# Kernel tuning notes

Measured on AMD Instinct MI355X. Metric: run time of the kernel, lower is better.

## Reference

```python
import jax, jax.numpy as jnp
import numpy as np

SHIFTS = (1, 2)          # _GLOBAL_SHIFTS, all < channels so none filtered
LN_EPS = 1e-5


def _layernorm(x, g, b):
    mu = jnp.mean(x, axis=-1, keepdims=True)
    var = jnp.var(x, axis=-1, keepdims=True)
    return (x - mu) * jax.lax.rsqrt(var + LN_EPS) * g + b


def setup_inputs() -> dict:
    key = jax.random.key(0)
    ks = jax.random.split(key, 4)
    B, H, W, D = 8, 96, 96, 256
    n_comp = 2 * len(SHIFTS)  # full mode: dot + wedge per shift
    x = jax.random.normal(ks[0], (B, H, W, D), dtype=jnp.float32)
    # glorot-uniform style scaling for the two dense kernels
    pk = jax.random.normal(ks[1], (n_comp * D, D), dtype=jnp.float32) * (1.0 / np.sqrt(n_comp * D))
    gk = jax.random.normal(ks[2], (2 * D, D), dtype=jnp.float32) * (1.0 / np.sqrt(2 * D))
    return {
        "x": x,
        "ln_gamma": jnp.ones((D,), jnp.float32),
        "ln_beta": jnp.zeros((D,), jnp.float32),
        "proj_kernel": pk,
        "proj_bias": jnp.zeros((D,), jnp.float32),
        "gate_kernel": gk,
        "gate_bias": jnp.zeros((D,), jnp.float32),
        "gamma": jnp.full((D,), 1e-5, jnp.float32),  # LayerScale init
    }


def reference(x, ln_gamma, ln_beta, proj_kernel, proj_bias,
              gate_kernel, gate_bias, gamma):
    # ---- pre-norm ----
    h_norm = _layernorm(x, ln_gamma, ln_beta)                 # [B,H,W,D]
    # ---- context stream (ctx_mode='diff'): deviation from spatial mean ----
    z_det = h_norm
    z_ctx = h_norm - jnp.mean(h_norm, axis=(1, 2), keepdims=True)
    # ---- sparse rolling Clifford product (cli_mode='full') ----
    feats = []
    for s in SHIFTS:
        ctx_s = jnp.roll(z_ctx, -s, axis=-1)   # Z_ctx[(c+s) % D]
        det_s = jnp.roll(z_det, -s, axis=-1)   # Z_det[(c+s) % D]
        dot = jax.nn.silu(z_det * ctx_s)                      # inner part
        wedge = z_det * ctx_s - z_ctx * det_s                 # bivector part
        feats.append(dot)
        feats.append(wedge)
    feats = jnp.concatenate(feats, axis=-1)                   # [B,H,W,4D]
    g_feat = feats @ proj_kernel + proj_bias                  # [B,H,W,D]
    # ---- gated geometric residual ----
    gate_in = jnp.concatenate([h_norm, g_feat], axis=-1)      # [B,H,W,2D]
    alpha = jax.nn.sigmoid(gate_in @ gate_kernel + gate_bias)
    h_mix = (jax.nn.silu(h_norm) + alpha * g_feat) * gamma    # LayerScale
    # drop_path_rate == 0.0 -> identity; caller-side residual add
    return x + h_mix
```

## Files before the change

kernel.cpp:

```cpp
#include <hip/hip_runtime.h>
#include <hip/hip_bf16.h>

typedef unsigned short u16;
typedef unsigned int   u32;
typedef __attribute__((ext_vector_type(4))) float f32x4;
typedef __attribute__((ext_vector_type(4))) u32   u32x4;
typedef __attribute__((ext_vector_type(8))) short bf16x8;

#define HWPIX  9216
#define NPIX   73728
#define LN_EPS 1e-5f
#define MROW   64
#define HSTR   264
#define ASTR   40

template<int N> struct IC { static constexpr int value = N; };

__device__ __forceinline__ u16 f2bf(float f){
  u32 u = __builtin_bit_cast(u32, f);
  u += 0x7fffu + ((u >> 16) & 1u);
  return (u16)(u >> 16);
}
__device__ __forceinline__ u32 pkbf(float lo, float hi){
  u32 d;
  asm("v_cvt_pk_bf16_f32 %0, %1, %2" : "=v"(d) : "v"(lo), "v"(hi));
  return d;
}
__device__ __forceinline__ float lo2f(u32 w){ return __builtin_bit_cast(float, w << 16); }
__device__ __forceinline__ float hi2f(u32 w){ return __builtin_bit_cast(float, w & 0xffff0000u); }
__device__ __forceinline__ float bfu2f(u16 h){ return __builtin_bit_cast(float, (u32)h << 16); }
__device__ __forceinline__ float fsigmoid(float v){ return __fdividef(1.f, 1.f + __expf(-v)); }
__device__ __forceinline__ float fsilu(float v){ return __fdividef(v, 1.f + __expf(-v)); }

__global__ __launch_bounds__(256) void wconv(const float* __restrict__ pk,
                                             const float* __restrict__ gk,
                                             u16* __restrict__ wsdot,
                                             u16* __restrict__ wsgate)
{
  int gid = blockIdx.x * 256 + threadIdx.x;
  int t = gid >> 10, S = gid & 1023;
  int q = (S >> 2) & 15, pp = S & 3, w8 = (S >> 6) & 7, rb = S >> 9;
  int n  = rb * 128 + w8 * 16 + q;
  int kq = pp ^ ((q >> 1) & 3);
  const float* W; int k0; u16* dst;
  if (t < 8)       { W = pk; k0 =       t      * 32 + kq * 8; dst = wsdot  + (size_t)t * 8192; }
  else if (t < 16) { W = pk; k0 = 512 + (t-8)  * 32 + kq * 8; dst = wsdot  + (size_t)t * 8192; }
  else             { W = gk; k0 =       (t-16) * 32 + kq * 8; dst = wsgate + (size_t)(t-16) * 8192; }
  u32 ow[4];
  #pragma unroll
  for (int e = 0; e < 4; ++e) {
    float f0 = W[(size_t)(k0 + 2*e)     * 256 + n];
    float f1 = W[(size_t)(k0 + 2*e + 1) * 256 + n];
    ow[e] = (u32)f2bf(f0) | ((u32)f2bf(f1) << 16);
  }
  *(u32x4*)(dst + (size_t)S * 8) = (u32x4){ow[0], ow[1], ow[2], ow[3]};
}

__global__ __launch_bounds__(256) void ln_partial(const float* __restrict__ x,
                                                  const float* __restrict__ g,
                                                  const float* __restrict__ bt,
                                                  float* __restrict__ partial)
{
  const int bh = blockIdx.x;
  const int tid = threadIdx.x;
  const int wv = tid >> 6, lane = tid & 63;
  const float* xrow = x + (size_t)bh * 96 * 256;
  __shared__ float red[4][256];

  f32x4 gv = *(const f32x4*)(g  + lane * 4);
  f32x4 bv = *(const f32x4*)(bt + lane * 4);
  f32x4 acc = {0.f, 0.f, 0.f, 0.f};

  for (int w = wv; w < 96; w += 4) {
    f32x4 v = *(const f32x4*)(xrow + w * 256 + lane * 4);
    float s  = v[0] + v[1] + v[2] + v[3];
    float s2 = v[0]*v[0] + v[1]*v[1] + v[2]*v[2] + v[3]*v[3];
    #pragma unroll
    for (int m = 1; m < 64; m <<= 1) { s += __shfl_xor(s, m); s2 += __shfl_xor(s2, m); }
    float mu  = s * (1.f / 256.f);
    float var = s2 * (1.f / 256.f) - mu * mu;
    float rs  = rsqrtf(var + LN_EPS);
    #pragma unroll
    for (int j = 0; j < 4; ++j) acc[j] += (v[j] - mu) * rs * gv[j] + bv[j];
  }
  *(f32x4*)(&red[wv][lane * 4]) = acc;
  __syncthreads();
  float s = red[0][tid] + red[1][tid] + red[2][tid] + red[3][tid];
  partial[(size_t)bh * 256 + tid] = s;
}

__global__ __launch_bounds__(256) void ln_mean(const float* __restrict__ partial,
                                               float* __restrict__ mean)
{
  int b = blockIdx.x, c = threadIdx.x;
  float s = 0.f;
  for (int h = 0; h < 96; ++h) s += partial[((size_t)b * 96 + h) * 256 + c];
  float m = s * (1.f / 9216.f);
  mean[b * 258 + c] = m;
  if (c < 2) mean[b * 258 + 256 + c] = m;
}

__global__ __launch_bounds__(256) void wfold(const float* __restrict__ pk,
                                             const float* __restrict__ meang,
                                             u16* __restrict__ wsW)
{
  __shared__ float msh[256];
  int gid = blockIdx.x * 256 + threadIdx.x;
  int chunk = gid >> 10;
  int b = chunk >> 3, j = chunk & 7;
  msh[threadIdx.x] = meang[b * 258 + threadIdx.x];
  __syncthreads();
  int S = gid & 1023;
  int q = (S >> 2) & 15, pp = S & 3, w8 = (S >> 6) & 7, rb = S >> 9;
  int n  = rb * 128 + w8 * 16 + q;
  int kq = pp ^ ((q >> 1) & 3);
  u32 ow[4];
  #pragma unroll
  for (int e = 0; e < 4; ++e) {
    float r[2];
    #pragma unroll
    for (int hh = 0; hh < 2; ++hh) {
      int c = j * 32 + kq * 8 + 2 * e + hh;
      int cm1 = (c + 255) & 255, cm2 = (c + 254) & 255;
      int cp1 = (c + 1) & 255,   cp2 = (c + 2) & 255;
      r[hh] = msh[cm1] * pk[(size_t)(256 + cm1) * 256 + n]
            - msh[cp1] * pk[(size_t)(256 + c)   * 256 + n]
            + msh[cm2] * pk[(size_t)(768 + cm2) * 256 + n]
            - msh[cp2] * pk[(size_t)(768 + c)   * 256 + n];
    }
    ow[e] = (u32)f2bf(r[0]) | ((u32)f2bf(r[1]) << 16);
  }
  *(u32x4*)(wsW + (size_t)chunk * 8192 + (size_t)S * 8) = (u32x4){ow[0], ow[1], ow[2], ow[3]};
}

__global__ __launch_bounds__(512, 4) void fused(
    const float* __restrict__ x,
    const float* __restrict__ lng, const float* __restrict__ lnb,
    const u16* __restrict__ wsdot, const u16* __restrict__ wsW,
    const u16* __restrict__ wsgate,
    const float* __restrict__ pbias, const float* __restrict__ gbias,
    const float* __restrict__ gamma, const float* __restrict__ meang,
    float* __restrict__ out)
{
  __shared__ u16 hn[MROW * HSTR];
  __shared__ u16 afg[2][MROW * ASTR];
  __shared__ u16 Bl [2][8192];
  __shared__ float msh[258];

  const int tid  = threadIdx.x;
  const long pix0 = (long)blockIdx.x * MROW;
  const int bat  = (int)(pix0 / HWPIX);

  if (tid < 258) msh[tid] = meang[bat * 258 + tid];

  const int wave = tid >> 6, lane = tid & 63;
  const int wr = wave & 1, wc = wave >> 1;
  const int fr = lane & 15, kq = lane >> 4;
  const int bswz = (kq ^ ((fr >> 1) & 3)) * 8;
  const int br = tid >> 3, bo = (tid & 7) * 4;

  f32x4 acc[2][4];
  #pragma unroll
  for (int i = 0; i < 2; ++i)
    #pragma unroll
    for (int j = 0; j < 4; ++j) acc[i][j] = (f32x4){0.f, 0.f, 0.f, 0.f};
  u32 gfp[2][4][2];
  float pbv[4];
  #pragma unroll
  for (int nt = 0; nt < 4; ++nt) pbv[nt] = pbias[wc * 64 + nt * 16 + fr];

  u32x4 breg0, breg1;
  auto sgptr = [&](auto SG) -> const u16* {
    constexpr int sg = decltype(SG)::value;
    if constexpr      (sg == 0) return wsdot;
    else if constexpr (sg == 1) return wsdot + 8 * 8192;
    else if constexpr (sg == 2) return wsW + (size_t)bat * 65536;
    else if constexpr (sg == 3) return wsgate;
    else                        return wsgate + 8 * 8192;
  };
  auto loadB = [&](auto SG, int jn) {
    const u16* src = sgptr(SG) + (size_t)jn * 8192 + tid * 8;
    breg0 = *(const u32x4*)(src);
    breg1 = *(const u32x4*)(src + 4096);
  };
  auto writeB = [&](int buf) {
    *(u32x4*)(&Bl[buf][tid * 8])        = breg0;
    *(u32x4*)(&Bl[buf][tid * 8 + 4096]) = breg1;
  };

  loadB(IC<0>{}, 0);

  {
    const int p = tid >> 3, o = tid & 7;
    const float* xp = x + (pix0 + p) * 256 + o * 32;
    f32x4 v[8];
    float s = 0.f, s2 = 0.f;
    #pragma unroll
    for (int i = 0; i < 8; ++i) {
      v[i] = *(const f32x4*)(xp + i * 4);
      #pragma unroll
      for (int j = 0; j < 4; ++j) { s += v[i][j]; s2 += v[i][j] * v[i][j]; }
    }
    s += __shfl_xor(s, 1); s2 += __shfl_xor(s2, 1);
    s += __shfl_xor(s, 2); s2 += __shfl_xor(s2, 2);
    s += __shfl_xor(s, 4); s2 += __shfl_xor(s2, 4);
    float mu  = s * (1.f / 256.f);
    float var = s2 * (1.f / 256.f) - mu * mu;
    float rs  = rsqrtf(var + LN_EPS);

    const float* gp = lng + o * 32;
    const float* bp = lnb + o * 32;
    u16* zd = hn + p * HSTR + o * 32;
    u32 pad_d = 0;
    #pragma unroll
    for (int i = 0; i < 8; ++i) {
      f32x4 gg = *(const f32x4*)(gp + i * 4);
      f32x4 bb = *(const f32x4*)(bp + i * 4);
      float h0 = (v[i][0] - mu) * rs * gg[0] + bb[0];
      float h1 = (v[i][1] - mu) * rs * gg[1] + bb[1];
      float h2 = (v[i][2] - mu) * rs * gg[2] + bb[2];
      float h3 = (v[i][3] - mu) * rs * gg[3] + bb[3];
      u32 d0 = pkbf(h0, h1);
      u32 d1 = pkbf(h2, h3);
      *(u32*)(zd + i * 4)     = d0;
      *(u32*)(zd + i * 4 + 2) = d1;
      if (i == 0) pad_d = d0;
    }
    if (o == 0) *(u32*)(hn + p * HSTR + 256) = pad_d;
  }

  auto featsD = [&](auto SC, int w, int buf) {
    constexpr int s = decltype(SC)::value;
    const int cc = w * 32 + bo;
    const u16* zp = hn + br * HSTR + cc;
    u32 a0 = *(const u32*)(zp);
    u32 a1 = *(const u32*)(zp + 2);
    u32 a2 = *(const u32*)(zp + 4);
    float h0 = lo2f(a0), h1 = hi2f(a0), h2 = lo2f(a1);
    float h3 = hi2f(a1), h4 = lo2f(a2), h5 = hi2f(a2);
    float m0 = msh[cc + s], m1 = msh[cc + s + 1];
    float m2 = msh[cc + s + 2], m3 = msh[cc + s + 3];
    float t0, t1, t2, t3;
    if constexpr (s == 1) { t0 = h1; t1 = h2; t2 = h3; t3 = h4; }
    else                  { t0 = h2; t1 = h3; t2 = h4; t3 = h5; }
    float r0 = fsilu(h0 * (t0 - m0));
    float r1 = fsilu(h1 * (t1 - m1));
    float r2 = fsilu(h2 * (t2 - m2));
    float r3 = fsilu(h3 * (t3 - m3));
    *(u32*)(&afg[buf][br * ASTR + bo])     = pkbf(r0, r1);
    *(u32*)(&afg[buf][br * ASTR + bo + 2]) = pkbf(r2, r3);
  };

  auto gfcopy = [&](auto CGC, int buf) {
    constexpr int cg = decltype(CGC)::value;
    constexpr int par = cg & 1;
    if (wc == (cg >> 1)) {
      #pragma unroll
      for (int v = 0; v < 2; ++v) {
        #pragma unroll
        for (int ai = 0; ai < 2; ++ai)
          #pragma unroll
          for (int rp = 0; rp < 2; ++rp) {
            u32 pw = gfp[ai][par * 2 + v][rp];
            int row0 = wr * 32 + ai * 16 + kq * 4 + rp * 2;
            afg[buf][row0 * ASTR + v * 16 + fr]       = (u16)pw;
            afg[buf][(row0 + 1) * ASTR + v * 16 + fr] = (u16)(pw >> 16);
          }
      }
    }
  };

  auto domfma = [&](const u16* abase, int astr, int buf) {
    bf16x8 av0 = *(const bf16x8*)(abase);
    bf16x8 av1 = *(const bf16x8*)(abase + 16 * astr);
    const u16* bp = &Bl[buf][wc * 2048 + fr * 32 + bswz];
    #pragma unroll
    for (int nt = 0; nt < 4; ++nt) {
      bf16x8 bv = *(const bf16x8*)(bp + nt * 512);
      acc[0][nt] = __builtin_amdgcn_mfma_f32_16x16x32_bf16(av0, bv, acc[0][nt], 0, 0, 0);
      acc[1][nt] = __builtin_amdgcn_mfma_f32_16x16x32_bf16(av1, bv, acc[1][nt], 0, 0, 0);
    }
  };

  __syncthreads();
  writeB(0);
  featsD(IC<1>{}, 0, 0);
  __syncthreads();

  auto stepfn = [&](auto SEGC, auto JC) {
    constexpr int SEG = decltype(SEGC)::value;
    constexpr int j   = decltype(JC)::value;
    constexpr int t   = SEG * 8 + j;
    constexpr int cb  = t & 1, nb = cb ^ 1;
    constexpr int u   = t + 1;
    constexpr int useg = (j == 7) ? SEG + 1 : SEG;
    constexpr int uj   = u & 7;
    if constexpr (u < 40) loadB(IC<useg>{}, uj);
    if constexpr      (useg == 0) featsD(IC<1>{}, uj, nb);
    else if constexpr (useg == 1) featsD(IC<2>{}, uj, nb);
    else if constexpr (useg == 4 && u < 40) gfcopy(IC<u - 32>{}, nb);
    if constexpr (SEG == 0 || SEG == 1 || SEG == 4)
      domfma(&afg[cb][(wr * 32 + fr) * ASTR + kq * 8], ASTR, cb);
    else
      domfma(&hn[(wr * 32 + fr) * HSTR + j * 32 + kq * 8], HSTR, cb);
    if constexpr (t == 23) {
      #pragma unroll
      for (int nt = 0; nt < 4; ++nt)
        #pragma unroll
        for (int ai = 0; ai < 2; ++ai) {
          f32x4 a = acc[ai][nt];
          gfp[ai][nt][0] = pkbf(a[0] + pbv[nt], a[1] + pbv[nt]);
          gfp[ai][nt][1] = pkbf(a[2] + pbv[nt], a[3] + pbv[nt]);
          acc[ai][nt] = (f32x4){0.f, 0.f, 0.f, 0.f};
        }
    }
    if constexpr (u < 40) writeB(nb);
    __syncthreads();
  };
  auto runseg = [&](auto SEGC) {
    stepfn(SEGC, IC<0>{}); stepfn(SEGC, IC<1>{});
    stepfn(SEGC, IC<2>{}); stepfn(SEGC, IC<3>{});
    stepfn(SEGC, IC<4>{}); stepfn(SEGC, IC<5>{});
    stepfn(SEGC, IC<6>{}); stepfn(SEGC, IC<7>{});
  };
  runseg(IC<0>{}); runseg(IC<1>{}); runseg(IC<2>{});
  runseg(IC<3>{}); runseg(IC<4>{});

  float gbv[4], gmv[4];
  #pragma unroll
  for (int nt = 0; nt < 4; ++nt) {
    int col = wc * 64 + nt * 16 + fr;
    gbv[nt] = gbias[col]; gmv[nt] = gamma[col];
  }
  #pragma unroll
  for (int ai = 0; ai < 2; ++ai)
    #pragma unroll
    for (int rr = 0; rr < 4; ++rr) {
      const int row = wr * 32 + ai * 16 + kq * 4 + rr;
      const long pix = pix0 + row;
      #pragma unroll
      for (int nt = 0; nt < 4; ++nt) {
        int col = wc * 64 + nt * 16 + fr;
        float xv = x[pix * 256 + col];
        float hh = bfu2f(hn[row * HSTR + col]);
        u32 pw = gfp[ai][nt][rr >> 1];
        float gfv = bfu2f((u16)((rr & 1) ? (pw >> 16) : pw));
        float al = fsigmoid(acc[ai][nt][rr] + gbv[nt]);
        out[pix * 256 + col] = xv + (fsilu(hh) + al * gfv) * gmv[nt];
      }
    }
}

extern "C" void kernel_launch(void* const* d_in, const int* in_sizes, int n_in,
                              void* d_out, int out_size, void* d_ws, size_t ws_size,
                              hipStream_t stream) {
  const float* x     = (const float*)d_in[0];
  const float* lng   = (const float*)d_in[1];
  const float* lnb   = (const float*)d_in[2];
  const float* pk    = (const float*)d_in[3];
  const float* pbias = (const float*)d_in[4];
  const float* gk    = (const float*)d_in[5];
  const float* gbias = (const float*)d_in[6];
  const float* gamma = (const float*)d_in[7];
  float* out = (float*)d_out;

  char* ws = (char*)d_ws;
  u16*   wsdot   = (u16*)ws;
  u16*   wsgate  = (u16*)(ws + 262144);
  float* meang   = (float*)(ws + 524288);
  u16*   wsW     = (u16*)(ws + 532544);
  float* partial = (float*)(ws + 532544);

  wconv<<<128, 256, 0, stream>>>(pk, gk, wsdot, wsgate);
  ln_partial<<<768, 256, 0, stream>>>(x, lng, lnb, partial);
  ln_mean<<<8, 256, 0, stream>>>(partial, meang);
  wfold<<<256, 256, 0, stream>>>(pk, meang, wsW);
  fused<<<NPIX / MROW, 512, 0, stream>>>(x, lng, lnb, wsdot, wsW, wsgate,
                                         pbias, gbias, gamma, meang, out);
}
```

Before: 165.7 us.

## Deepen B-tile global prefetch to two steps with dual register sets

Weight tiles are now fetched two steps ahead into alternating register sets, and the LDS write for the next buffer is moved before the MFMA block instead of after it. The aim is to hide global-load latency behind a full step of MFMA work. The layernorm also re-reads x from global (cache) instead of keeping eight vectors live, which frees registers to pay for the extra prefetch registers. The trade-offs are more register pressure from the second set and a duplicate read of x.

```diff
diff --git a/kernel.cpp b/kernel.cpp
--- a/kernel.cpp
+++ b/kernel.cpp
@@ -151,8 +151,6 @@
   const long pix0 = (long)blockIdx.x * MROW;
   const int bat  = (int)(pix0 / HWPIX);
 
-  if (tid < 258) msh[tid] = meang[bat * 258 + tid];
-
   const int wave = tid >> 6, lane = tid & 63;
   const int wr = wave & 1, wc = wave >> 1;
   const int fr = lane & 15, kq = lane >> 4;
@@ -165,11 +163,8 @@
     #pragma unroll
     for (int j = 0; j < 4; ++j) acc[i][j] = (f32x4){0.f, 0.f, 0.f, 0.f};
   u32 gfp[2][4][2];
-  float pbv[4];
-  #pragma unroll
-  for (int nt = 0; nt < 4; ++nt) pbv[nt] = pbias[wc * 64 + nt * 16 + fr];
-
-  u32x4 breg0, breg1;
+
+  u32x4 brA0, brA1, brB0, brB1;
   auto sgptr = [&](auto SG) -> const u16* {
     constexpr int sg = decltype(SG)::value;
     if constexpr      (sg == 0) return wsdot;
@@ -178,28 +173,44 @@
     else if constexpr (sg == 3) return wsgate;
     else                        return wsgate + 8 * 8192;
   };
-  auto loadB = [&](auto SG, int jn) {
+  auto loadB = [&](auto SG, int jn, auto SET) {
     const u16* src = sgptr(SG) + (size_t)jn * 8192 + tid * 8;
-    breg0 = *(const u32x4*)(src);
-    breg1 = *(const u32x4*)(src + 4096);
-  };
-  auto writeB = [&](int buf) {
-    *(u32x4*)(&Bl[buf][tid * 8])        = breg0;
-    *(u32x4*)(&Bl[buf][tid * 8 + 4096]) = breg1;
-  };
-
-  loadB(IC<0>{}, 0);
+    if constexpr (decltype(SET)::value == 0) {
+      brA0 = *(const u32x4*)(src);
+      brA1 = *(const u32x4*)(src + 4096);
+    } else {
+      brB0 = *(const u32x4*)(src);
+      brB1 = *(const u32x4*)(src + 4096);
+    }
+  };
+  auto writeB = [&](auto SET, int buf) {
+    if constexpr (decltype(SET)::value == 0) {
+      *(u32x4*)(&Bl[buf][tid * 8])        = brA0;
+      *(u32x4*)(&Bl[buf][tid * 8 + 4096]) = brA1;
+    } else {
+      *(u32x4*)(&Bl[buf][tid * 8])        = brB0;
+      *(u32x4*)(&Bl[buf][tid * 8 + 4096]) = brB1;
+    }
+  };
+
+  loadB(IC<0>{}, 0, IC<0>{});
+  loadB(IC<0>{}, 1, IC<1>{});
+
+  if (tid < 258) msh[tid] = meang[bat * 258 + tid];
+
+  float pbv[4];
+  #pragma unroll
+  for (int nt = 0; nt < 4; ++nt) pbv[nt] = pbias[wc * 64 + nt * 16 + fr];
 
   {
     const int p = tid >> 3, o = tid & 7;
     const float* xp = x + (pix0 + p) * 256 + o * 32;
-    f32x4 v[8];
     float s = 0.f, s2 = 0.f;
     #pragma unroll
     for (int i = 0; i < 8; ++i) {
-      v[i] = *(const f32x4*)(xp + i * 4);
-      #pragma unroll
-      for (int j = 0; j < 4; ++j) { s += v[i][j]; s2 += v[i][j] * v[i][j]; }
+      f32x4 v = *(const f32x4*)(xp + i * 4);
+      s  += v[0] + v[1] + v[2] + v[3];
+      s2 += v[0]*v[0] + v[1]*v[1] + v[2]*v[2] + v[3]*v[3];
     }
     s += __shfl_xor(s, 1); s2 += __shfl_xor(s2, 1);
     s += __shfl_xor(s, 2); s2 += __shfl_xor(s2, 2);
@@ -211,22 +222,21 @@
     const float* gp = lng + o * 32;
     const float* bp = lnb + o * 32;
     u16* zd = hn + p * HSTR + o * 32;
-    u32 pad_d = 0;
     #pragma unroll
     for (int i = 0; i < 8; ++i) {
+      f32x4 v  = *(const f32x4*)(xp + i * 4);
       f32x4 gg = *(const f32x4*)(gp + i * 4);
       f32x4 bb = *(const f32x4*)(bp + i * 4);
-      float h0 = (v[i][0] - mu) * rs * gg[0] + bb[0];
-      float h1 = (v[i][1] - mu) * rs * gg[1] + bb[1];
-      float h2 = (v[i][2] - mu) * rs * gg[2] + bb[2];
-      float h3 = (v[i][3] - mu) * rs * gg[3] + bb[3];
+      float h0 = (v[0] - mu) * rs * gg[0] + bb[0];
+      float h1 = (v[1] - mu) * rs * gg[1] + bb[1];
+      float h2 = (v[2] - mu) * rs * gg[2] + bb[2];
+      float h3 = (v[3] - mu) * rs * gg[3] + bb[3];
       u32 d0 = pkbf(h0, h1);
       u32 d1 = pkbf(h2, h3);
       *(u32*)(zd + i * 4)     = d0;
       *(u32*)(zd + i * 4 + 2) = d1;
-      if (i == 0) pad_d = d0;
-    }
-    if (o == 0) *(u32*)(hn + p * HSTR + 256) = pad_d;
+      if (i == 0 && o == 0) *(u32*)(hn + p * HSTR + 256) = d0;
+    }
   }
 
   auto featsD = [&](auto SC, int w, int buf) {
@@ -283,7 +293,7 @@
   };
 
   __syncthreads();
-  writeB(0);
+  writeB(IC<0>{}, 0);
   featsD(IC<1>{}, 0, 0);
   __syncthreads();
 
@@ -292,13 +302,16 @@
     constexpr int j   = decltype(JC)::value;
     constexpr int t   = SEG * 8 + j;
     constexpr int cb  = t & 1, nb = cb ^ 1;
-    constexpr int u   = t + 1;
-    constexpr int useg = (j == 7) ? SEG + 1 : SEG;
-    constexpr int uj   = u & 7;
-    if constexpr (u < 40) loadB(IC<useg>{}, uj);
-    if constexpr      (useg == 0) featsD(IC<1>{}, uj, nb);
-    else if constexpr (useg == 1) featsD(IC<2>{}, uj, nb);
-    else if constexpr (useg == 4 && u < 40) gfcopy(IC<u - 32>{}, nb);
+    constexpr int l   = t + 2;
+    if constexpr (l < 40) loadB(IC<(l >> 3)>{}, l & 7, IC<l & 1>{});
+    constexpr int u    = t + 1;
+    constexpr int useg = u >> 3;
+    if constexpr (u < 40) {
+      if constexpr      (useg == 0) featsD(IC<1>{}, u & 7, nb);
+      else if constexpr (useg == 1) featsD(IC<2>{}, u & 7, nb);
+      else if constexpr (useg == 4) gfcopy(IC<u - 32>{}, nb);
+      writeB(IC<u & 1>{}, nb);
+    }
     if constexpr (SEG == 0 || SEG == 1 || SEG == 4)
       domfma(&afg[cb][(wr * 32 + fr) * ASTR + kq * 8], ASTR, cb);
     else
@@ -314,7 +327,6 @@
           acc[ai][nt] = (f32x4){0.f, 0.f, 0.f, 0.f};
         }
     }
-    if constexpr (u < 40) writeB(nb);
     __syncthreads();
   };
   auto runseg = [&](auto SEGC) {
```

Result: faster. 158.5 us (-4.3%).
